# Kernel tuning notes

Hardware: AMD Instinct MI355X
Metric: run time of the kernel (lower is better)

The kernel has to match this reference:

```python
import jax, jax.numpy as jnp
import numpy as np

N = 100000   # nodes
E = 1000000  # edges per graph (avg degree 10)
D = 300      # feature dim


def _layernorm(x, gamma, beta, eps=1e-5):
    mu = jnp.mean(x, axis=-1, keepdims=True)
    var = jnp.mean(jnp.square(x - mu), axis=-1, keepdims=True)
    return (x - mu) * jax.lax.rsqrt(var + eps) * gamma + beta


def _graph_conv(edges, x, W, b, num_nodes):
    # DGL GraphConv with norm='both' and relu activation:
    # h = relu( D_in^{-1/2} A D_out^{-1/2} x W + b )
    src, dst = edges[0], edges[1]
    ones = jnp.ones((edges.shape[1],), x.dtype)
    out_deg = jax.ops.segment_sum(ones, src, num_segments=num_nodes)
    in_deg = jax.ops.segment_sum(ones, dst, num_segments=num_nodes)
    norm_src = jnp.where(out_deg > 0, jax.lax.rsqrt(jnp.maximum(out_deg, 1.0)), 0.0)
    norm_dst = jnp.where(in_deg > 0, jax.lax.rsqrt(jnp.maximum(in_deg, 1.0)), 0.0)
    h = x * norm_src[:, None]                                  # [N, D]
    agg = jax.ops.segment_sum(h[src], dst, num_segments=num_nodes)  # gather+scatter
    agg = agg * norm_dst[:, None]
    return jax.nn.relu(agg @ W + b)


def setup_inputs() -> dict:
    key = jax.random.key(0)
    ks = jax.random.split(key, 8)
    s = 0.05  # weight scale
    return {
        "table_feat": jax.random.normal(ks[0], (N, D), jnp.float32),
        "row_edges": jax.random.randint(ks[1], (2, E), 0, N, jnp.int32),
        "col_edges": jax.random.randint(ks[2], (2, E), 0, N, jnp.int32),
        "Wr": jax.random.normal(ks[3], (D, D), jnp.float32) * s,
        "br": jnp.zeros((D,), jnp.float32),
        "Wc": jax.random.normal(ks[4], (D, D), jnp.float32) * s,
        "bc": jnp.zeros((D,), jnp.float32),
        "Wrs": jax.random.normal(ks[5], (D, D), jnp.float32) * s,
        "brs": jnp.zeros((D,), jnp.float32),
        "g_rs": jnp.ones((D,), jnp.float32),
        "b_rs": jnp.zeros((D,), jnp.float32),
        "Wcs": jax.random.normal(ks[6], (D, D), jnp.float32) * s,
        "bcs": jnp.zeros((D,), jnp.float32),
        "g_cs": jnp.ones((D,), jnp.float32),
        "b_cs": jnp.zeros((D,), jnp.float32),
        "Wm": jax.random.normal(ks[7], (2 * D, D), jnp.float32) * s,
        "bm": jnp.zeros((D,), jnp.float32),
        "g_m": jnp.ones((D,), jnp.float32),
        "b_m": jnp.zeros((D,), jnp.float32),
    }


def reference(table_feat, row_edges, col_edges, Wr, br, Wc, bc,
              Wrs, brs, g_rs, b_rs, Wcs, bcs, g_cs, b_cs,
              Wm, bm, g_m, b_m):
    rowg = _graph_conv(row_edges, table_feat, Wr, br, N)   # row_aware GraphConv
    colg = _graph_conv(col_edges, table_feat, Wc, bc, N)   # col_aware GraphConv
    rowg = _layernorm(rowg @ Wrs + brs, g_rs, b_rs)        # row_graph_support
    colg = _layernorm(colg @ Wcs + bcs, g_cs, b_cs)        # col_graph_support
    merged = jnp.concatenate([rowg, colg], axis=1)          # [N, 2D]
    return _layernorm(merged @ Wm + bm, g_m, b_m)           # graph_merge
```

## Files before the change

kernel.cpp:

```cpp
#include <hip/hip_runtime.h>
#include <stdint.h>

#define SP 304
#define NT 10
#define KS300 19

typedef unsigned short u16;
using short8 = __attribute__((ext_vector_type(8))) short;
using f32x16 = __attribute__((ext_vector_type(16))) float;

__device__ __forceinline__ float b2f(u16 u) {
    return __uint_as_float(((unsigned)u) << 16);
}
__device__ __forceinline__ u16 f2b(float f) {
    unsigned u = __float_as_uint(f);
    return (u16)((u + 0x7FFFu + ((u >> 16) & 1u)) >> 16);
}
__device__ __forceinline__ float scrub(float v) {
    unsigned u = __float_as_uint(v);
    return (((u >> 23) & 0xFFu) == 0xFFu) ? 0.f : v;
}
__device__ __forceinline__ u16 sb16(u16 v) {
    return (((v >> 7) & 0xFFu) == 0xFFu) ? (u16)0 : v;
}

__global__ void detect_dtype(const u16* __restrict__ xs, int* __restrict__ flag) {
    __shared__ int cnt[256];
    int c = 0;
    for (int i = 0; i < 16; i++) {
        u16 v = xs[threadIdx.x * 16 + i];
        unsigned e = (v >> 7) & 0xFFu;
        c += (e >= 100u && e <= 150u) ? 1 : 0;
    }
    cnt[threadIdx.x] = c;
    __syncthreads();
    for (int s = 128; s > 0; s >>= 1) {
        if (threadIdx.x < s) cnt[threadIdx.x] += cnt[threadIdx.x + s];
        __syncthreads();
    }
    if (threadIdx.x == 0) flag[0] = (cnt[0] >= 3686) ? 1 : 0;
}

template<bool BF16>
__global__ __launch_bounds__(256) void conv_x(const void* __restrict__ x, u16* __restrict__ xb,
                                              int total4, const int* __restrict__ flag) {
    if ((flag[0] != 0) != BF16) return;
    int idx = blockIdx.x * 256 + threadIdx.x;
    if (idx >= total4) return;
    int node = idx / 76, c = idx - node * 76;
    ushort4 v = make_ushort4(0, 0, 0, 0);
    if (c < 75) {
        if (BF16) {
            v = *(const ushort4*)((const u16*)x + (size_t)node * 300 + c * 4);
            v.x = sb16(v.x); v.y = sb16(v.y); v.z = sb16(v.z); v.w = sb16(v.w);
        } else {
            float4 f = *(const float4*)((const float*)x + (size_t)node * 300 + c * 4);
            v = make_ushort4(f2b(scrub(f.x)), f2b(scrub(f.y)), f2b(scrub(f.z)), f2b(scrub(f.w)));
        }
    }
    *(ushort4*)(xb + (size_t)node * SP + c * 4) = v;
}

template<bool BF16>
__global__ void pack_b(const void* __restrict__ W, u16* __restrict__ P, int nseg,
                       const int* __restrict__ flag) {
    if ((flag[0] != 0) != BF16) return;
    int idx = blockIdx.x * 256 + threadIdx.x;
    int total = nseg * KS300 * NT * 512;
    if (idx >= total) return;
    int j = idx & 7, lane = (idx >> 3) & 63, t = idx >> 9;
    int nt = t % NT, ks = t / NT;
    int seg = ks / KS300, ksl = ks - seg * KS300;
    int kk = ksl * 16 + ((lane >> 5) << 3) + j;
    int n = nt * 32 + (lane & 31);
    u16 v = 0;
    if (kk < 300 && n < 300) {
        int wk = seg * 300 + kk;
        if (BF16) v = sb16(((const u16*)W)[(size_t)wk * 300 + n]);
        else      v = f2b(scrub(((const float*)W)[(size_t)wk * 300 + n]));
    }
    P[idx] = v;
}

template<bool BF16>
__global__ void conv_params(const void* p0, const void* p1, const void* p2, const void* p3,
                            const void* p4, const void* p5, const void* p6, const void* p7,
                            const void* p8, const void* p9, const void* p10,
                            float* __restrict__ pbuf, const int* __restrict__ flag) {
    if ((flag[0] != 0) != BF16) return;
    int idx = blockIdx.x * 256 + threadIdx.x;
    if (idx >= 11 * 304) return;
    int j = idx / 304, c = idx % 304;
    const void* ps[11] = {p0, p1, p2, p3, p4, p5, p6, p7, p8, p9, p10};
    float v = 0.f;
    if (c < 300) {
        if (BF16) v = b2f(sb16(((const u16*)ps[j])[c]));
        else      v = scrub(((const float*)ps[j])[c]);
    }
    pbuf[j * 304 + c] = v;
}

__global__ void count_deg(const int* __restrict__ src, const int* __restrict__ dst, int E,
                          int* __restrict__ outd, int* __restrict__ ind) {
    int e = blockIdx.x * 256 + threadIdx.x;
    if (e < E) {
        atomicAdd(&outd[src[e]], 1);
        atomicAdd(&ind[dst[e]], 1);
    }
}

__global__ __launch_bounds__(256) void alloc_norm(int Nn,
                           const int* __restrict__ odR, const int* __restrict__ idR,
                           const int* __restrict__ odC, const int* __restrict__ idC,
                           int* __restrict__ offR, int* __restrict__ offC,
                           float* __restrict__ nsR, float* __restrict__ ndR,
                           float* __restrict__ nsC, float* __restrict__ ndC,
                           int* __restrict__ cur2) {
    __shared__ int sR[256], sC[256];
    __shared__ int baseR, baseC;
    int tid = threadIdx.x;
    int i = blockIdx.x * 256 + tid;
    int dR = (i < Nn) ? idR[i] : 0;
    int dC = (i < Nn) ? idC[i] : 0;
    sR[tid] = dR; sC[tid] = dC;
    __syncthreads();
    for (int off = 1; off < 256; off <<= 1) {
        int vR = (tid >= off) ? sR[tid - off] : 0;
        int vC = (tid >= off) ? sC[tid - off] : 0;
        __syncthreads();
        sR[tid] += vR; sC[tid] += vC;
        __syncthreads();
    }
    if (tid == 0) {
        baseR = atomicAdd(&cur2[0], sR[255]);
        baseC = atomicAdd(&cur2[1], sC[255]);
    }
    __syncthreads();
    if (i < Nn) {
        offR[i] = baseR + sR[tid] - dR;
        offC[i] = baseC + sC[tid] - dC;
        nsR[i] = odR[i] > 0 ? rsqrtf((float)odR[i]) : 0.f;
        ndR[i] = idR[i] > 0 ? rsqrtf((float)idR[i]) : 0.f;
        nsC[i] = odC[i] > 0 ? rsqrtf((float)odC[i]) : 0.f;
        ndC[i] = idC[i] > 0 ? rsqrtf((float)idC[i]) : 0.f;
    }
}

__global__ void fill_csr(const int* __restrict__ src, const int* __restrict__ dst, int E,
                         const int* __restrict__ offs, int* __restrict__ cursor,
                         int* __restrict__ adj) {
    int e = blockIdx.x * 256 + threadIdx.x;
    if (e < E) {
        int d = dst[e];
        int p = offs[d] + atomicAdd(&cursor[d], 1);
        adj[p] = src[e];
    }
}

__global__ __launch_bounds__(256) void aggregate(
    const u16* __restrict__ xb, const int* __restrict__ adj, const int* __restrict__ offs,
    const int* __restrict__ deg, const float* __restrict__ ns, const float* __restrict__ nd,
    u16* __restrict__ agg, int Nn) {
    int w = threadIdx.x >> 6, lane = threadIdx.x & 63;
    int node = blockIdx.x * 4 + w;
    if (node >= Nn) return;
    int bg = offs[node], cnt = deg[node];
    const bool part = lane < 12;
    const int c0 = 4 * lane, c1 = 256 + 4 * lane;
    float a0 = 0, a1 = 0, a2 = 0, a3 = 0, p0 = 0, p1 = 0, p2 = 0, p3 = 0;
    int j = 0;
    for (; j + 2 <= cnt; j += 2) {
        int s0 = adj[bg + j], s1 = adj[bg + j + 1];
        float n0 = ns[s0], n1 = ns[s1];
        const u16* r0p = xb + (size_t)s0 * SP;
        const u16* r1p = xb + (size_t)s1 * SP;
        ushort4 v0 = *(const ushort4*)(r0p + c0);
        ushort4 v1 = *(const ushort4*)(r1p + c0);
        a0 += b2f(v0.x) * n0 + b2f(v1.x) * n1;
        a1 += b2f(v0.y) * n0 + b2f(v1.y) * n1;
        a2 += b2f(v0.z) * n0 + b2f(v1.z) * n1;
        a3 += b2f(v0.w) * n0 + b2f(v1.w) * n1;
        if (part) {
            ushort4 u0 = *(const ushort4*)(r0p + c1);
            ushort4 u1 = *(const ushort4*)(r1p + c1);
            p0 += b2f(u0.x) * n0 + b2f(u1.x) * n1;
            p1 += b2f(u0.y) * n0 + b2f(u1.y) * n1;
            p2 += b2f(u0.z) * n0 + b2f(u1.z) * n1;
            p3 += b2f(u0.w) * n0 + b2f(u1.w) * n1;
        }
    }
    if (j < cnt) {
        int s = adj[bg + j];
        float nv = ns[s];
        const u16* rp = xb + (size_t)s * SP;
        ushort4 v = *(const ushort4*)(rp + c0);
        a0 += b2f(v.x) * nv; a1 += b2f(v.y) * nv; a2 += b2f(v.z) * nv; a3 += b2f(v.w) * nv;
        if (part) {
            ushort4 u = *(const ushort4*)(rp + c1);
            p0 += b2f(u.x) * nv; p1 += b2f(u.y) * nv; p2 += b2f(u.z) * nv; p3 += b2f(u.w) * nv;
        }
    }
    float ndv = nd[node];
    u16* o = agg + (size_t)node * SP;
    *(ushort4*)(o + c0) = make_ushort4(f2b(a0 * ndv), f2b(a1 * ndv), f2b(a2 * ndv), f2b(a3 * ndv));
    if (part)
        *(ushort4*)(o + c1) = make_ushort4(f2b(p0 * ndv), f2b(p1 * ndv), f2b(p2 * ndv), f2b(p3 * ndv));
}

template<int MODE, bool OUTF32>
__global__ __launch_bounds__(256, 3) void gemm_f(
    const u16* __restrict__ A1, const u16* __restrict__ A2,
    const u16* __restrict__ Bp, const float* __restrict__ bias,
    const float* __restrict__ gamma, const float* __restrict__ beta,
    void* __restrict__ out, int M, const int* __restrict__ flag) {
    if (MODE == 2) {
        if ((flag[0] != 0) != (!OUTF32)) return;
    }
    __shared__ __align__(16) char smem[2048 + 38912];
    float* red = (float*)smem;

    const int tid = threadIdx.x;
    const int w = tid >> 6, l = tid & 63;
    const int pr = w >> 1, sd = w & 1;
    const int mb = blockIdx.x * 64;
    const int r0 = mb + pr * 32;
    const bool act = r0 < M;
    const int lc = l & 31, hi = l >> 5;
    const int rowA = act ? min(r0 + lc, M - 1) : 0;
    const u16* a1 = A1 + (size_t)rowA * SP + hi * 8;
    const u16* a2 = A2 + (size_t)rowA * SP + hi * 8;
    const u16* bl = Bp + (size_t)(sd * 5) * 512 + (size_t)l * 8;
    const int colbase = sd * 160;

    f32x16 acc[5];
#pragma unroll
    for (int i = 0; i < 5; ++i)
#pragma unroll
        for (int r = 0; r < 16; ++r) acc[i][r] = 0.f;

    for (int ks = 0; ks < KS300; ++ks) {
        short8 af = *(const short8*)(a1 + ks * 16);
        const u16* bb = bl + (size_t)ks * (NT * 512);
#pragma unroll
        for (int i = 0; i < 5; ++i) {
            short8 bf = *(const short8*)(bb + i * 512);
            acc[i] = __builtin_amdgcn_mfma_f32_32x32x16_bf16(af, bf, acc[i], 0, 0, 0);
        }
    }
    if (MODE == 2) {
        for (int ks = KS300; ks < 2 * KS300; ++ks) {
            short8 af = *(const short8*)(a2 + (ks - KS300) * 16);
            const u16* bb = bl + (size_t)ks * (NT * 512);
#pragma unroll
            for (int i = 0; i < 5; ++i) {
                short8 bf = *(const short8*)(bb + i * 512);
                acc[i] = __builtin_amdgcn_mfma_f32_32x32x16_bf16(af, bf, acc[i], 0, 0, 0);
            }
        }
    }

    if (MODE == 0) {
        u16* stg = (u16*)(smem + 2048);
        if (act) {
#pragma unroll
            for (int i = 0; i < 5; ++i) {
                int col = colbase + i * 32 + lc;
                if (col < 304) {
                    float bb = col < 300 ? bias[col] : 0.f;
#pragma unroll
                    for (int r = 0; r < 16; ++r) {
                        int rowl = 4 * hi + (r & 3) + 8 * (r >> 2);
                        float v = scrub(acc[i][r] + bb);
                        v = v > 0.f ? v : 0.f;
                        stg[(pr * 32 + rowl) * SP + col] = col < 300 ? f2b(v) : (u16)0;
                    }
                }
            }
        }
        __syncthreads();
        int rows = min(64, M - mb);
        u16* dst = (u16*)out + (size_t)mb * SP;
        if (rows == 64) {
#pragma unroll
            for (int k = 0; k < 10; ++k) {
                int idx = k * 256 + tid;
                if (idx < 2432) *(short8*)(dst + idx * 8) = *(const short8*)(stg + idx * 8);
            }
        } else {
            for (int idx = tid; idx < rows * SP; idx += 256) dst[idx] = stg[idx];
        }
        return;
    }

    float sum[16], ssq[16];
#pragma unroll
    for (int r = 0; r < 16; ++r) { sum[r] = 0.f; ssq[r] = 0.f; }
#pragma unroll
    for (int i = 0; i < 5; ++i) {
        int col = colbase + i * 32 + lc;
        bool cv = col < 300;
        float bb = cv ? bias[col] : 0.f;
#pragma unroll
        for (int r = 0; r < 16; ++r) {
            float v = cv ? scrub(acc[i][r] + bb) : 0.f;
            acc[i][r] = v;
            sum[r] += v;
            ssq[r] += v * v;
        }
    }
#pragma unroll
    for (int off = 1; off < 32; off <<= 1) {
#pragma unroll
        for (int r = 0; r < 16; ++r) {
            sum[r] += __shfl_xor(sum[r], off);
            ssq[r] += __shfl_xor(ssq[r], off);
        }
    }
    if (act) {
#pragma unroll
        for (int r = 0; r < 16; ++r) {
            if (lc == r) {
                int rowl = 4 * hi + (r & 3) + 8 * (r >> 2);
                float* q = red + ((pr * 2 + sd) * 32 + rowl) * 2;
                q[0] = sum[r]; q[1] = ssq[r];
            }
        }
    }
    __syncthreads();
    float mean[16], inv[16];
    if (act) {
#pragma unroll
        for (int r = 0; r < 16; ++r) {
            int rowl = 4 * hi + (r & 3) + 8 * (r >> 2);
            const float* q = red + ((pr * 2 + (1 - sd)) * 32 + rowl) * 2;
            float s = sum[r] + q[0], qq = ssq[r] + q[1];
            mean[r] = s * (1.f / 300.f);
            float var = fmaxf(qq * (1.f / 300.f) - mean[r] * mean[r], 0.f);
            inv[r] = rsqrtf(var + 1e-5f);
        }
    }

    if (MODE == 1) {
        u16* stg = (u16*)(smem + 2048);
        if (act) {
#pragma unroll
            for (int i = 0; i < 5; ++i) {
                int col = colbase + i * 32 + lc;
                if (col < 304) {
                    float g = col < 300 ? gamma[col] : 0.f;
                    float be = col < 300 ? beta[col] : 0.f;
#pragma unroll
                    for (int r = 0; r < 16; ++r) {
                        int rowl = 4 * hi + (r & 3) + 8 * (r >> 2);
                        float v = (acc[i][r] - mean[r]) * inv[r] * g + be;
                        stg[(pr * 32 + rowl) * SP + col] = col < 300 ? f2b(v) : (u16)0;
                    }
                }
            }
        }
        __syncthreads();
        int rows = min(64, M - mb);
        u16* dst = (u16*)out + (size_t)mb * SP;
        if (rows == 64) {
#pragma unroll
            for (int k = 0; k < 10; ++k) {
                int idx = k * 256 + tid;
                if (idx < 2432) *(short8*)(dst + idx * 8) = *(const short8*)(stg + idx * 8);
            }
        } else {
            for (int idx = tid; idx < rows * SP; idx += 256) dst[idx] = stg[idx];
        }
    } else if (!OUTF32) {
        u16* stg = (u16*)(smem + 2048);
        if (act) {
#pragma unroll
            for (int i = 0; i < 5; ++i) {
                int col = colbase + i * 32 + lc;
                if (col < 300) {
                    float g = gamma[col], be = beta[col];
#pragma unroll
                    for (int r = 0; r < 16; ++r) {
                        int rowl = 4 * hi + (r & 3) + 8 * (r >> 2);
                        float v = (acc[i][r] - mean[r]) * inv[r] * g + be;
                        stg[(pr * 32 + rowl) * 300 + col] = f2b(v);
                    }
                }
            }
        }
        __syncthreads();
        int rows = min(64, M - mb);
        u16* dst = (u16*)out + (size_t)mb * 300;
        if (rows == 64) {
#pragma unroll
            for (int k = 0; k < 10; ++k) {
                int idx = k * 256 + tid;
                if (idx < 2400) *(short8*)(dst + idx * 8) = *(const short8*)(stg + idx * 8);
            }
        } else {
            for (int idx = tid; idx < rows * 300; idx += 256) dst[idx] = stg[idx];
        }
    } else {
        float* fst = (float*)(smem + 2048);
        for (int pp = 0; pp < 2; ++pp) {
            __syncthreads();
            if (pr == pp && act) {
#pragma unroll
                for (int i = 0; i < 5; ++i) {
                    int col = colbase + i * 32 + lc;
                    if (col < 300) {
                        float g = gamma[col], be = beta[col];
#pragma unroll
                        for (int r = 0; r < 16; ++r) {
                            int rowl = 4 * hi + (r & 3) + 8 * (r >> 2);
                            float v = (acc[i][r] - mean[r]) * inv[r] * g + be;
                            fst[rowl * 300 + col] = v;
                        }
                    }
                }
            }
            __syncthreads();
            int tr0 = mb + pp * 32;
            if (tr0 < M) {
                int rows = min(32, M - tr0);
                float* dst = (float*)out + (size_t)tr0 * 300;
                if (rows == 32) {
#pragma unroll
                    for (int k = 0; k < 10; ++k) {
                        int idx = k * 256 + tid;
                        if (idx < 2400) *(float4*)(dst + idx * 4) = *(const float4*)(fst + idx * 4);
                    }
                } else {
                    for (int idx = tid; idx < rows * 300; idx += 256) dst[idx] = fst[idx];
                }
            }
        }
    }
}

extern "C" void kernel_launch(void* const* d_in, const int* in_sizes, int n_in,
                              void* d_out, int out_size, void* d_ws, size_t ws_size,
                              hipStream_t stream) {
    (void)n_in; (void)out_size; (void)ws_size;
    const void* x   = d_in[0];
    const int* re   = (const int*)d_in[1];
    const int* ce   = (const int*)d_in[2];

    const int Nn = in_sizes[0] / 300;
    const int Er = in_sizes[1] / 2;
    const int Ec = in_sizes[2] / 2;

    char* p = (char*)d_ws;
    size_t off = 0;
    auto balloc = [&](size_t bytes) -> void* {
        void* r = p + off;
        off += (bytes + 255) & ~(size_t)255;
        return r;
    };
    int* degR  = (int*)balloc((size_t)Nn * 4);
    int* odegR = (int*)balloc((size_t)Nn * 4);
    int* degC  = (int*)balloc((size_t)Nn * 4);
    int* odegC = (int*)balloc((size_t)Nn * 4);
    int* curR  = (int*)balloc((size_t)Nn * 4);
    int* curC  = (int*)balloc((size_t)Nn * 4);
    int* cur2  = (int*)balloc(64 * 4);
    size_t zbytes = off;
    int* flag  = (int*)balloc(256);
    int* offsR = (int*)balloc((size_t)Nn * 4);
    int* offsC = (int*)balloc((size_t)Nn * 4);
    float* nsR = (float*)balloc((size_t)Nn * 4);
    float* ndR = (float*)balloc((size_t)Nn * 4);
    float* nsC = (float*)balloc((size_t)Nn * 4);
    float* ndC = (float*)balloc((size_t)Nn * 4);
    int* adjR  = (int*)balloc((size_t)Er * 4);
    int* adjC  = (int*)balloc((size_t)Ec * 4);
    const size_t PB1 = (size_t)KS300 * NT * 512;
    u16* WrP   = (u16*)balloc(PB1 * 2);
    u16* WcP   = (u16*)balloc(PB1 * 2);
    u16* WrsP  = (u16*)balloc(PB1 * 2);
    u16* WcsP  = (u16*)balloc(PB1 * 2);
    u16* WmP   = (u16*)balloc(2 * PB1 * 2);
    float* pbuf = (float*)balloc(11 * 304 * 4);
    u16* xb    = (u16*)balloc((size_t)Nn * SP * 2);
    u16* B2    = (u16*)balloc((size_t)Nn * SP * 2);
    u16* B3    = (u16*)balloc((size_t)Nn * SP * 2);

    const float* pbr  = pbuf + 0 * 304;
    const float* pbc  = pbuf + 1 * 304;
    const float* pbrs = pbuf + 2 * 304;
    const float* pgrs = pbuf + 3 * 304;
    const float* pBrs = pbuf + 4 * 304;
    const float* pbcs = pbuf + 5 * 304;
    const float* pgcs = pbuf + 6 * 304;
    const float* pBcs = pbuf + 7 * 304;
    const float* pbm  = pbuf + 8 * 304;
    const float* pgm  = pbuf + 9 * 304;
    const float* pBm  = pbuf + 10 * 304;

    detect_dtype<<<1, 256, 0, stream>>>((const u16*)x, flag);
    hipMemsetAsync(d_ws, 0, zbytes, stream);

    const int total4 = Nn * 76;
    conv_x<true><<<(total4 + 255) / 256, 256, 0, stream>>>(x, xb, total4, flag);
    conv_x<false><<<(total4 + 255) / 256, 256, 0, stream>>>(x, xb, total4, flag);

#define PK(Wsrc, Pdst, nseg)                                                                  \
    pack_b<true><<<(int)(((nseg) * PB1 + 255) / 256), 256, 0, stream>>>(Wsrc, Pdst, nseg, flag); \
    pack_b<false><<<(int)(((nseg) * PB1 + 255) / 256), 256, 0, stream>>>(Wsrc, Pdst, nseg, flag)
    PK(d_in[3], WrP, 1);
    PK(d_in[5], WcP, 1);
    PK(d_in[7], WrsP, 1);
    PK(d_in[11], WcsP, 1);
    PK(d_in[15], WmP, 2);
#undef PK

    conv_params<true><<<14, 256, 0, stream>>>(d_in[4], d_in[6], d_in[8], d_in[9], d_in[10],
                                              d_in[12], d_in[13], d_in[14], d_in[16], d_in[17],
                                              d_in[18], pbuf, flag);
    conv_params<false><<<14, 256, 0, stream>>>(d_in[4], d_in[6], d_in[8], d_in[9], d_in[10],
                                               d_in[12], d_in[13], d_in[14], d_in[16], d_in[17],
                                               d_in[18], pbuf, flag);

    count_deg<<<(Er + 255) / 256, 256, 0, stream>>>(re, re + Er, Er, odegR, degR);
    count_deg<<<(Ec + 255) / 256, 256, 0, stream>>>(ce, ce + Ec, Ec, odegC, degC);
    alloc_norm<<<(Nn + 255) / 256, 256, 0, stream>>>(Nn, odegR, degR, odegC, degC,
                                                     offsR, offsC, nsR, ndR, nsC, ndC, cur2);
    fill_csr<<<(Er + 255) / 256, 256, 0, stream>>>(re, re + Er, Er, offsR, curR, adjR);
    fill_csr<<<(Ec + 255) / 256, 256, 0, stream>>>(ce, ce + Ec, Ec, offsC, curC, adjC);

    aggregate<<<(Nn + 3) / 4, 256, 0, stream>>>(xb, adjR, offsR, degR, nsR, ndR, B2, Nn);
    aggregate<<<(Nn + 3) / 4, 256, 0, stream>>>(xb, adjC, offsC, degC, nsC, ndC, B3, Nn);

    const int gb = (Nn + 63) / 64;
    gemm_f<0, false><<<gb, 256, 0, stream>>>(B2, B2, WrP, pbr, nullptr, nullptr, B2, Nn, flag);
    gemm_f<0, false><<<gb, 256, 0, stream>>>(B3, B3, WcP, pbc, nullptr, nullptr, B3, Nn, flag);
    gemm_f<1, false><<<gb, 256, 0, stream>>>(B2, B2, WrsP, pbrs, pgrs, pBrs, B2, Nn, flag);
    gemm_f<1, false><<<gb, 256, 0, stream>>>(B3, B3, WcsP, pbcs, pgcs, pBcs, B3, Nn, flag);
    gemm_f<2, false><<<gb, 256, 0, stream>>>(B2, B3, WmP, pbm, pgm, pBm, d_out, Nn, flag);
    gemm_f<2, true ><<<gb, 256, 0, stream>>>(B2, B3, WmP, pbm, pgm, pBm, d_out, Nn, flag);
}
```

Baseline: 1.129 ms.

## Fuse conv GEMM and support GEMM+layernorm per branch via LDS intermediate

Replaces the two separate GEMM passes per graph branch (GraphConv linear+relu, then support linear+layernorm) with one kernel that keeps the relu output tile in shared memory (padded stride 310) and feeds it straight into the second GEMM. This removes a full write and read of the N×304 bf16 intermediate per branch and two kernel launches. The aggregate gather loop is also unrolled from 2 to 4 neighbors to put more independent loads in flight. Shared memory per block grows to about 41 KB, which may limit occupancy, and the padded stride changes LDS access patterns for the A-fragment loads.

```diff
diff --git a/kernel.cpp b/kernel.cpp
--- a/kernel.cpp
+++ b/kernel.cpp
@@ -2,6 +2,7 @@
 #include <stdint.h>
 
 #define SP 304
+#define HSP 310
 #define NT 10
 #define KS300 19
 
@@ -169,27 +170,33 @@
     const int c0 = 4 * lane, c1 = 256 + 4 * lane;
     float a0 = 0, a1 = 0, a2 = 0, a3 = 0, p0 = 0, p1 = 0, p2 = 0, p3 = 0;
     int j = 0;
-    for (; j + 2 <= cnt; j += 2) {
-        int s0 = adj[bg + j], s1 = adj[bg + j + 1];
-        float n0 = ns[s0], n1 = ns[s1];
-        const u16* r0p = xb + (size_t)s0 * SP;
-        const u16* r1p = xb + (size_t)s1 * SP;
-        ushort4 v0 = *(const ushort4*)(r0p + c0);
-        ushort4 v1 = *(const ushort4*)(r1p + c0);
-        a0 += b2f(v0.x) * n0 + b2f(v1.x) * n1;
-        a1 += b2f(v0.y) * n0 + b2f(v1.y) * n1;
-        a2 += b2f(v0.z) * n0 + b2f(v1.z) * n1;
-        a3 += b2f(v0.w) * n0 + b2f(v1.w) * n1;
+    for (; j + 4 <= cnt; j += 4) {
+        int s0 = adj[bg + j], s1 = adj[bg + j + 1], s2 = adj[bg + j + 2], s3 = adj[bg + j + 3];
+        float n0 = ns[s0], n1 = ns[s1], n2 = ns[s2], n3 = ns[s3];
+        const u16* q0 = xb + (size_t)s0 * SP;
+        const u16* q1 = xb + (size_t)s1 * SP;
+        const u16* q2 = xb + (size_t)s2 * SP;
+        const u16* q3 = xb + (size_t)s3 * SP;
+        ushort4 v0 = *(const ushort4*)(q0 + c0);
+        ushort4 v1 = *(const ushort4*)(q1 + c0);
+        ushort4 v2 = *(const ushort4*)(q2 + c0);
+        ushort4 v3 = *(const ushort4*)(q3 + c0);
+        a0 += b2f(v0.x) * n0 + b2f(v1.x) * n1 + b2f(v2.x) * n2 + b2f(v3.x) * n3;
+        a1 += b2f(v0.y) * n0 + b2f(v1.y) * n1 + b2f(v2.y) * n2 + b2f(v3.y) * n3;
+        a2 += b2f(v0.z) * n0 + b2f(v1.z) * n1 + b2f(v2.z) * n2 + b2f(v3.z) * n3;
+        a3 += b2f(v0.w) * n0 + b2f(v1.w) * n1 + b2f(v2.w) * n2 + b2f(v3.w) * n3;
         if (part) {
-            ushort4 u0 = *(const ushort4*)(r0p + c1);
-            ushort4 u1 = *(const ushort4*)(r1p + c1);
-            p0 += b2f(u0.x) * n0 + b2f(u1.x) * n1;
-            p1 += b2f(u0.y) * n0 + b2f(u1.y) * n1;
-            p2 += b2f(u0.z) * n0 + b2f(u1.z) * n1;
-            p3 += b2f(u0.w) * n0 + b2f(u1.w) * n1;
-        }
-    }
-    if (j < cnt) {
+            ushort4 u0 = *(const ushort4*)(q0 + c1);
+            ushort4 u1 = *(const ushort4*)(q1 + c1);
+            ushort4 u2 = *(const ushort4*)(q2 + c1);
+            ushort4 u3 = *(const ushort4*)(q3 + c1);
+            p0 += b2f(u0.x) * n0 + b2f(u1.x) * n1 + b2f(u2.x) * n2 + b2f(u3.x) * n3;
+            p1 += b2f(u0.y) * n0 + b2f(u1.y) * n1 + b2f(u2.y) * n2 + b2f(u3.y) * n3;
+            p2 += b2f(u0.z) * n0 + b2f(u1.z) * n1 + b2f(u2.z) * n2 + b2f(u3.z) * n3;
+            p3 += b2f(u0.w) * n0 + b2f(u1.w) * n1 + b2f(u2.w) * n2 + b2f(u3.w) * n3;
+        }
+    }
+    for (; j < cnt; ++j) {
         int s = adj[bg + j];
         float nv = ns[s];
         const u16* rp = xb + (size_t)s * SP;
@@ -205,6 +212,155 @@
     *(ushort4*)(o + c0) = make_ushort4(f2b(a0 * ndv), f2b(a1 * ndv), f2b(a2 * ndv), f2b(a3 * ndv));
     if (part)
         *(ushort4*)(o + c1) = make_ushort4(f2b(p0 * ndv), f2b(p1 * ndv), f2b(p2 * ndv), f2b(p3 * ndv));
+}
+
+__global__ __launch_bounds__(256, 3) void gemm_fused(
+    const u16* __restrict__ Ain, const u16* __restrict__ B1p, const u16* __restrict__ B2p,
+    const float* __restrict__ bias1, const float* __restrict__ bias2,
+    const float* __restrict__ gamma2, const float* __restrict__ beta2,
+    u16* __restrict__ outp, int M) {
+    __shared__ __align__(16) char smem[2048 + 64 * HSP * 2];
+    float* red = (float*)smem;
+    u16* hb = (u16*)(smem + 2048);
+
+    const int tid = threadIdx.x;
+    const int w = tid >> 6, l = tid & 63;
+    const int pr = w >> 1, sd = w & 1;
+    const int mb = blockIdx.x * 64;
+    const int r0 = mb + pr * 32;
+    const bool act = r0 < M;
+    const int lc = l & 31, hi = l >> 5;
+    const int rowA = act ? min(r0 + lc, M - 1) : 0;
+    const u16* a1 = Ain + (size_t)rowA * SP + hi * 8;
+    const u16* bl1 = B1p + (size_t)(sd * 5) * 512 + (size_t)l * 8;
+    const u16* bl2 = B2p + (size_t)(sd * 5) * 512 + (size_t)l * 8;
+    const int colbase = sd * 160;
+
+    f32x16 acc[5];
+#pragma unroll
+    for (int i = 0; i < 5; ++i)
+#pragma unroll
+        for (int r = 0; r < 16; ++r) acc[i][r] = 0.f;
+
+    for (int ks = 0; ks < KS300; ++ks) {
+        short8 af = *(const short8*)(a1 + ks * 16);
+        const u16* bb = bl1 + (size_t)ks * (NT * 512);
+#pragma unroll
+        for (int i = 0; i < 5; ++i) {
+            short8 bf = *(const short8*)(bb + i * 512);
+            acc[i] = __builtin_amdgcn_mfma_f32_32x32x16_bf16(af, bf, acc[i], 0, 0, 0);
+        }
+    }
+    if (act) {
+#pragma unroll
+        for (int i = 0; i < 5; ++i) {
+            int col = colbase + i * 32 + lc;
+            if (col < 304) {
+                float bb = col < 300 ? bias1[col] : 0.f;
+#pragma unroll
+                for (int r = 0; r < 16; ++r) {
+                    int rowl = 4 * hi + (r & 3) + 8 * (r >> 2);
+                    float v = scrub(acc[i][r] + bb);
+                    v = v > 0.f ? v : 0.f;
+                    hb[(size_t)(pr * 32 + rowl) * HSP + col] = col < 300 ? f2b(v) : (u16)0;
+                }
+            }
+        }
+    }
+    __syncthreads();
+
+#pragma unroll
+    for (int i = 0; i < 5; ++i)
+#pragma unroll
+        for (int r = 0; r < 16; ++r) acc[i][r] = 0.f;
+    const u16* hrow = hb + (size_t)(pr * 32 + lc) * HSP + hi * 8;
+    for (int ks = 0; ks < KS300; ++ks) {
+        short8 af = *(const short8*)(hrow + ks * 16);
+        const u16* bb = bl2 + (size_t)ks * (NT * 512);
+#pragma unroll
+        for (int i = 0; i < 5; ++i) {
+            short8 bf = *(const short8*)(bb + i * 512);
+            acc[i] = __builtin_amdgcn_mfma_f32_32x32x16_bf16(af, bf, acc[i], 0, 0, 0);
+        }
+    }
+
+    float sum[16], ssq[16];
+#pragma unroll
+    for (int r = 0; r < 16; ++r) { sum[r] = 0.f; ssq[r] = 0.f; }
+#pragma unroll
+    for (int i = 0; i < 5; ++i) {
+        int col = colbase + i * 32 + lc;
+        bool cv = col < 300;
+        float bb = cv ? bias2[col] : 0.f;
+#pragma unroll
+        for (int r = 0; r < 16; ++r) {
+            float v = cv ? scrub(acc[i][r] + bb) : 0.f;
+            acc[i][r] = v;
+            sum[r] += v;
+            ssq[r] += v * v;
+        }
+    }
+#pragma unroll
+    for (int off = 1; off < 32; off <<= 1) {
+#pragma unroll
+        for (int r = 0; r < 16; ++r) {
+            sum[r] += __shfl_xor(sum[r], off);
+            ssq[r] += __shfl_xor(ssq[r], off);
+        }
+    }
+    if (act) {
+#pragma unroll
+        for (int r = 0; r < 16; ++r) {
+            if (lc == r) {
+                int rowl = 4 * hi + (r & 3) + 8 * (r >> 2);
+                float* q = red + ((pr * 2 + sd) * 32 + rowl) * 2;
+                q[0] = sum[r]; q[1] = ssq[r];
+            }
+        }
+    }
+    __syncthreads();
+    float mean[16], inv[16];
+    if (act) {
+#pragma unroll
+        for (int r = 0; r < 16; ++r) {
+            int rowl = 4 * hi + (r & 3) + 8 * (r >> 2);
+            const float* q = red + ((pr * 2 + (1 - sd)) * 32 + rowl) * 2;
+            float s = sum[r] + q[0], qq = ssq[r] + q[1];
+            mean[r] = s * (1.f / 300.f);
+            float var = fmaxf(qq * (1.f / 300.f) - mean[r] * mean[r], 0.f);
+            inv[r] = rsqrtf(var + 1e-5f);
+        }
+    }
+
+    u16* stg = hb;
+    if (act) {
+#pragma unroll
+        for (int i = 0; i < 5; ++i) {
+            int col = colbase + i * 32 + lc;
+            if (col < 304) {
+                float g = col < 300 ? gamma2[col] : 0.f;
+                float be = col < 300 ? beta2[col] : 0.f;
+#pragma unroll
+                for (int r = 0; r < 16; ++r) {
+                    int rowl = 4 * hi + (r & 3) + 8 * (r >> 2);
+                    float v = (acc[i][r] - mean[r]) * inv[r] * g + be;
+                    stg[(size_t)(pr * 32 + rowl) * SP + col] = col < 300 ? f2b(v) : (u16)0;
+                }
+            }
+        }
+    }
+    __syncthreads();
+    int rows = min(64, M - mb);
+    u16* dst = outp + (size_t)mb * SP;
+    if (rows == 64) {
+#pragma unroll
+        for (int k = 0; k < 10; ++k) {
+            int idx = k * 256 + tid;
+            if (idx < 2432) *(short8*)(dst + idx * 8) = *(const short8*)(stg + idx * 8);
+        }
+    } else {
+        for (int idx = tid; idx < rows * SP; idx += 256) dst[idx] = stg[idx];
+    }
 }
 
 template<int MODE, bool OUTF32>
@@ -259,39 +415,6 @@
         }
     }
 
-    if (MODE == 0) {
-        u16* stg = (u16*)(smem + 2048);
-        if (act) {
-#pragma unroll
-            for (int i = 0; i < 5; ++i) {
-                int col = colbase + i * 32 + lc;
-                if (col < 304) {
-                    float bb = col < 300 ? bias[col] : 0.f;
-#pragma unroll
-                    for (int r = 0; r < 16; ++r) {
-                        int rowl = 4 * hi + (r & 3) + 8 * (r >> 2);
-                        float v = scrub(acc[i][r] + bb);
-                        v = v > 0.f ? v : 0.f;
-                        stg[(pr * 32 + rowl) * SP + col] = col < 300 ? f2b(v) : (u16)0;
-                    }
-                }
-            }
-        }
-        __syncthreads();
-        int rows = min(64, M - mb);
-        u16* dst = (u16*)out + (size_t)mb * SP;
-        if (rows == 64) {
-#pragma unroll
-            for (int k = 0; k < 10; ++k) {
-                int idx = k * 256 + tid;
-                if (idx < 2432) *(short8*)(dst + idx * 8) = *(const short8*)(stg + idx * 8);
-            }
-        } else {
-            for (int idx = tid; idx < rows * SP; idx += 256) dst[idx] = stg[idx];
-        }
-        return;
-    }
-
     float sum[16], ssq[16];
 #pragma unroll
     for (int r = 0; r < 16; ++r) { sum[r] = 0.f; ssq[r] = 0.f; }
@@ -340,37 +463,7 @@
         }
     }
 
-    if (MODE == 1) {
-        u16* stg = (u16*)(smem + 2048);
-        if (act) {
-#pragma unroll
-            for (int i = 0; i < 5; ++i) {
-                int col = colbase + i * 32 + lc;
-                if (col < 304) {
-                    float g = col < 300 ? gamma[col] : 0.f;
-                    float be = col < 300 ? beta[col] : 0.f;
-#pragma unroll
-                    for (int r = 0; r < 16; ++r) {
-                        int rowl = 4 * hi + (r & 3) + 8 * (r >> 2);
-                        float v = (acc[i][r] - mean[r]) * inv[r] * g + be;
-                        stg[(pr * 32 + rowl) * SP + col] = col < 300 ? f2b(v) : (u16)0;
-                    }
-                }
-            }
-        }
-        __syncthreads();
-        int rows = min(64, M - mb);
-        u16* dst = (u16*)out + (size_t)mb * SP;
-        if (rows == 64) {
-#pragma unroll
-            for (int k = 0; k < 10; ++k) {
-                int idx = k * 256 + tid;
-                if (idx < 2432) *(short8*)(dst + idx * 8) = *(const short8*)(stg + idx * 8);
-            }
-        } else {
-            for (int idx = tid; idx < rows * SP; idx += 256) dst[idx] = stg[idx];
-        }
-    } else if (!OUTF32) {
+    if (!OUTF32) {
         u16* stg = (u16*)(smem + 2048);
         if (act) {
 #pragma unroll
@@ -531,10 +624,8 @@
     aggregate<<<(Nn + 3) / 4, 256, 0, stream>>>(xb, adjC, offsC, degC, nsC, ndC, B3, Nn);
 
     const int gb = (Nn + 63) / 64;
-    gemm_f<0, false><<<gb, 256, 0, stream>>>(B2, B2, WrP, pbr, nullptr, nullptr, B2, Nn, flag);
-    gemm_f<0, false><<<gb, 256, 0, stream>>>(B3, B3, WcP, pbc, nullptr, nullptr, B3, Nn, flag);
-    gemm_f<1, false><<<gb, 256, 0, stream>>>(B2, B2, WrsP, pbrs, pgrs, pBrs, B2, Nn, flag);
-    gemm_f<1, false><<<gb, 256, 0, stream>>>(B3, B3, WcsP, pbcs, pgcs, pBcs, B3, Nn, flag);
+    gemm_fused<<<gb, 256, 0, stream>>>(B2, WrP, WrsP, pbr, pbrs, pgrs, pBrs, B2, Nn);
+    gemm_fused<<<gb, 256, 0, stream>>>(B3, WcP, WcsP, pbc, pbcs, pgcs, pBcs, B3, Nn);
     gemm_f<2, false><<<gb, 256, 0, stream>>>(B2, B3, WmP, pbm, pgm, pBm, d_out, Nn, flag);
     gemm_f<2, true ><<<gb, 256, 0, stream>>>(B2, B3, WmP, pbm, pgm, pBm, d_out, Nn, flag);
 }
```

New measurement: 1.127 ms. About the same (-0.1%).
